# Kernel tuning notes

Hardware: AMD Instinct MI355X
Metric: run time of the kernel (lower is better)

The kernel has to match this reference:

```python
import jax, jax.numpy as jnp
import numpy as np
import math

H = 16
D_ATTN = 64
D_MID = 64
D_X = 1024
D_Z = 1024
D_OUT = 1024
B = 2
L_X = 2048
L_Z = 2048
MINUS_INFINITY = -1000000.0

def _xavier(key, shape):
    fan_in, fan_out = shape
    limit = math.sqrt(6.0 / (fan_in + fan_out))
    return jax.random.uniform(key, shape, jnp.float32, -limit, limit)

def setup_inputs() -> dict:
    key = jax.random.key(0)
    ks = jax.random.split(key, 8)
    primary = jax.random.normal(ks[0], (B, L_X, D_X), jnp.float32)
    context = jax.random.normal(ks[1], (B, L_Z, D_Z), jnp.float32)
    padding_mask = jnp.ones((B, L_Z), jnp.int32)
    # causal attention mask (b, l_x, l_z)
    attention_mask = jnp.broadcast_to(
        jnp.tril(jnp.ones((L_X, L_Z), jnp.int32))[None], (B, L_X, L_Z))
    W_qs = _xavier(ks[2], (D_X, H * D_ATTN))
    W_ks = _xavier(ks[3], (D_Z, H * D_ATTN))
    W_vs = _xavier(ks[4], (D_Z, H * D_MID))
    W_o = _xavier(ks[5], (H * D_MID, D_OUT))
    b_o = jnp.zeros((D_OUT,), jnp.float32)
    return {"primary": primary, "context": context,
            "padding_mask": padding_mask, "attention_mask": attention_mask,
            "W_qs": W_qs, "W_ks": W_ks, "W_vs": W_vs, "W_o": W_o, "b_o": b_o}

def reference(primary, context, padding_mask, attention_mask, W_qs, W_ks, W_vs, W_o, b_o):
    b, l_x, _ = primary.shape
    l_z = context.shape[1]
    # QKV projections, split into heads (head-major columns)
    q = (primary @ W_qs).reshape(b, l_x, H, D_ATTN).transpose(0, 2, 1, 3)  # (b,h,l_x,d_attn)
    k = (context @ W_ks).reshape(b, l_z, H, D_ATTN).transpose(0, 2, 1, 3)  # (b,h,l_z,d_attn)
    v = (context @ W_vs).reshape(b, l_z, H, D_MID).transpose(0, 2, 1, 3)   # (b,h,l_z,d_mid)
    scores = jnp.einsum('bhxd,bhzd->bhxz', q, k) / math.sqrt(D_ATTN)
    # combined mask: attention_mask AND padding_mask, broadcast over heads
    mask = (attention_mask * padding_mask[:, None, :])[:, None]  # (b,1,l_x,l_z)
    scores = jnp.where(mask == 0, MINUS_INFINITY, scores)
    attn = jax.nn.softmax(scores, axis=-1)
    out = jnp.einsum('bhxz,bhzm->bhxm', attn, v)  # (b,h,l_x,d_mid)
    out = out.transpose(0, 2, 1, 3).reshape(b, l_x, H * D_MID)
    return out @ W_o + b_o
```

## Files before the change

kernel.cpp:

```cpp
#include <hip/hip_runtime.h>

#define NB 2
#define LX 2048
#define LZ 2048
#define HH 16
#define DA 64
#define DM 64
#define HD 1024
#define MINF  -1000000.0f
#define QSC   0.1803368801f
#define DTHR  8.0f

typedef __attribute__((ext_vector_type(8))) short short8;
typedef __attribute__((ext_vector_type(4))) float f32x4;

static __device__ __forceinline__ ushort f2bf(float f) {
    union { float f; uint32_t u; } c; c.f = f;
    return (ushort)((c.u + 0x7FFFu + ((c.u >> 16) & 1u)) >> 16);
}

static __device__ __forceinline__ uint32_t cvtpk(float lo, float hi) {
    uint32_t r;
    asm("v_cvt_pk_bf16_f32 %0, %1, %2" : "=v"(r) : "v"(lo), "v"(hi));
    return r;
}

#define GL16(g, l) __builtin_amdgcn_global_load_lds( \
    (const __attribute__((address_space(1))) void*)(g), \
    (__attribute__((address_space(3))) void*)(l), 16, 0, 0)

__global__ __launch_bounds__(256) void cvt_both(
    const float* __restrict__ pA, const float* __restrict__ pB,
    ushort* __restrict__ oA, ushort* __restrict__ oB)
{
    const int i = blockIdx.x * 256 + threadIdx.x;
    const float* in = (i < 1048576) ? pA : pB;
    ushort* out = (i < 1048576) ? oA : oB;
    const int j = i & 1048575;
    float4 v = ((const float4*)in)[j];
    ushort4 o;
    o.x = f2bf(v.x); o.y = f2bf(v.y); o.z = f2bf(v.z); o.w = f2bf(v.w);
    ((ushort4*)out)[j] = o;
}

__global__ __launch_bounds__(256) void wtrans4(
    const float* __restrict__ W0, const float* __restrict__ W1,
    const float* __restrict__ W2, const float* __restrict__ W3,
    ushort* __restrict__ T0, ushort* __restrict__ T1,
    ushort* __restrict__ T2, ushort* __restrict__ T3)
{
    const int zz = blockIdx.z;
    const float* W = (zz == 0) ? W0 : (zz == 1) ? W1 : (zz == 2) ? W2 : W3;
    ushort* Wt = (zz == 0) ? T0 : (zz == 1) ? T1 : (zz == 2) ? T2 : T3;

    __shared__ ushort Ls[64][72];
    const int n0 = blockIdx.x * 64, k0 = blockIdx.y * 64;
    const int t = threadIdx.x;
    const int rr = t >> 4, c4 = (t & 15) * 4;
    #pragma unroll
    for (int i = 0; i < 4; ++i) {
        const int r = rr + i * 16;
        float4 v = *(const float4*)&W[(size_t)(k0 + r) * 1024 + n0 + c4];
        Ls[c4 + 0][r] = f2bf(v.x);
        Ls[c4 + 1][r] = f2bf(v.y);
        Ls[c4 + 2][r] = f2bf(v.z);
        Ls[c4 + 3][r] = f2bf(v.w);
    }
    __syncthreads();
    const int n = t >> 2, kc = (t & 3) * 16;
    *(short8*)&Wt[(size_t)(n0 + n) * 1024 + k0 + kc]     = *(const short8*)&Ls[n][kc];
    *(short8*)&Wt[(size_t)(n0 + n) * 1024 + k0 + kc + 8] = *(const short8*)&Ls[n][kc + 8];
}

template <bool OUTF32>
static __device__ __forceinline__ void gemm_body(
    const ushort* __restrict__ A, const ushort* __restrict__ Bt,
    const float* __restrict__ bias, void* __restrict__ Cout, float osc)
{
    __shared__ ushort As[128 * 32];
    __shared__ ushort Bs[128 * 32];
    const int t = threadIdx.x;
    const int w = t >> 6, l = t & 63, lr = l & 15, lg = l >> 4;
    const int wr = w >> 1, wc = w & 1;
    const int n0 = blockIdx.x * 128, m0 = blockIdx.y * 128;

    const int c0 = t, c1 = t + 256;
    const ushort* a0 = &A[(size_t)(m0 + (c0 >> 2)) * 1024 + (c0 & 3) * 8];
    const ushort* a1 = &A[(size_t)(m0 + (c1 >> 2)) * 1024 + (c1 & 3) * 8];
    const ushort* b0 = &Bt[(size_t)(n0 + (c0 >> 2)) * 1024 + (c0 & 3) * 8];
    const ushort* b1 = &Bt[(size_t)(n0 + (c1 >> 2)) * 1024 + (c1 & 3) * 8];
    ushort* lA0 = &As[w * 512];
    ushort* lA1 = &As[(4 + w) * 512];
    ushort* lB0 = &Bs[w * 512];
    ushort* lB1 = &Bs[(4 + w) * 512];

    f32x4 acc[4][4];
    #pragma unroll
    for (int i = 0; i < 4; ++i)
        #pragma unroll
        for (int j = 0; j < 4; ++j) acc[i][j] = 0.f;

    for (int k0 = 0; k0 < 1024; k0 += 32) {
        __syncthreads();
        GL16(a0 + k0, lA0);
        GL16(a1 + k0, lA1);
        GL16(b0 + k0, lB0);
        GL16(b1 + k0, lB1);
        __syncthreads();
        short8 af[4], bf[4];
        #pragma unroll
        for (int mi = 0; mi < 4; ++mi)
            af[mi] = *(const short8*)&As[(wr * 64 + mi * 16 + lr) * 32 + lg * 8];
        #pragma unroll
        for (int nj = 0; nj < 4; ++nj)
            bf[nj] = *(const short8*)&Bs[(wc * 64 + nj * 16 + lr) * 32 + lg * 8];
        #pragma unroll
        for (int mi = 0; mi < 4; ++mi)
            #pragma unroll
            for (int nj = 0; nj < 4; ++nj)
                acc[mi][nj] = __builtin_amdgcn_mfma_f32_16x16x32_bf16(
                    af[mi], bf[nj], acc[mi][nj], 0, 0, 0);
    }

    const int row0 = m0 + wr * 64, col0 = n0 + wc * 64;
    #pragma unroll
    for (int mi = 0; mi < 4; ++mi)
        #pragma unroll
        for (int nj = 0; nj < 4; ++nj) {
            const int col = col0 + nj * 16 + lr;
            #pragma unroll
            for (int r = 0; r < 4; ++r) {
                const int row = row0 + mi * 16 + lg * 4 + r;
                const float v = acc[mi][nj][r];
                if (OUTF32)
                    ((float*)Cout)[(size_t)row * 1024 + col] = v + bias[col];
                else
                    ((ushort*)Cout)[(size_t)row * 1024 + col] = f2bf(v * osc);
            }
        }
}

__global__ __launch_bounds__(256) void gemm_qkv(
    const ushort* __restrict__ Pb, const ushort* __restrict__ Cb,
    const ushort* __restrict__ Wqt, const ushort* __restrict__ Wkt,
    const ushort* __restrict__ Wvt,
    ushort* __restrict__ Qb, ushort* __restrict__ Kb, ushort* __restrict__ Vb)
{
    const int z = blockIdx.z;
    const ushort* A  = (z == 0) ? Pb : Cb;
    const ushort* Bt = (z == 0) ? Wqt : (z == 1) ? Wkt : Wvt;
    ushort* C = (z == 0) ? Qb : (z == 1) ? Kb : Vb;
    const float osc = (z == 0) ? QSC : 1.0f;
    gemm_body<false>(A, Bt, nullptr, C, osc);
}

__global__ __launch_bounds__(256) void gemm_out(
    const ushort* __restrict__ A, const ushort* __restrict__ Bt,
    const float* __restrict__ bias, float* __restrict__ Cout)
{
    gemm_body<true>(A, Bt, bias, Cout, 1.0f);
}

__global__ __launch_bounds__(256) void mask_classify(
    const int* __restrict__ amask, const int* __restrict__ pmask,
    int* __restrict__ cls)
{
    const int bid = blockIdx.x;
    const int b = bid >> 10, xb = (bid >> 5) & 31, zb = bid & 31;
    const int t = threadIdx.x;
    int andv = 1, orv = 0;
    #pragma unroll
    for (int i = 0; i < 16; ++i) {
        const int e = t + i * 256;
        const int r = e >> 6, z = e & 63;
        const int m = amask[((size_t)b * LX + xb * 64 + r) * LZ + zb * 64 + z];
        const int p = pmask[(size_t)b * LZ + zb * 64 + z];
        const int v = (m != 0) & (p != 0);
        andv &= v; orv |= v;
    }
    __shared__ int sa[256];
    __shared__ int so[256];
    sa[t] = andv; so[t] = orv;
    __syncthreads();
    for (int s = 128; s > 0; s >>= 1) {
        if (t < s) { sa[t] &= sa[t + s]; so[t] |= so[t + s]; }
        __syncthreads();
    }
    if (t == 0) cls[bid] = so[0] ? (sa[0] ? 1 : 2) : 0;
}

__global__ __launch_bounds__(256) void attn_mfma(
    const ushort* __restrict__ Qg, const ushort* __restrict__ Kg,
    const ushort* __restrict__ Vg, const int* __restrict__ amask,
    const int* __restrict__ pmask, const int* __restrict__ cls,
    ushort* __restrict__ O)
{
    __shared__ ushort Ks[64 * 72];
    __shared__ ushort Vt[64 * 64];

    const int t = threadIdx.x, w = t >> 6, l = t & 63, lr = l & 15, lg = l >> 4;
    const int x = blockIdx.x, h = blockIdx.y, b = blockIdx.z;
    const int fx = (x & 1) ? 15 - (x >> 1) : (x >> 1);
    const int qb = b ? 15 - fx : fx;
    const int qw = qb * 128 + w * 32;

    short8 qf[2][2];
    #pragma unroll
    for (int mi = 0; mi < 2; ++mi)
        #pragma unroll
        for (int ks = 0; ks < 2; ++ks)
            qf[mi][ks] = *(const short8*)&Qg[(size_t)(b * LX + qw + mi * 16 + lr) * HD
                                             + h * DA + ks * 32 + lg * 8];

    float mrun[2] = {-1e30f, -1e30f}, lrun[2] = {0.f, 0.f};
    f32x4 o[2][4];
    #pragma unroll
    for (int mi = 0; mi < 2; ++mi)
        #pragma unroll
        for (int mj = 0; mj < 4; ++mj) o[mi][mj] = 0.f;

    const int kz = t >> 2, kc = (t & 3) * 16;
    const int vz = (t >> 3) * 2, vc = (t & 7) * 8;

    for (int zb = 0; zb < LZ / 64; ++zb) {
        const int cls0 = cls[b * 1024 + (qb * 2) * 32 + zb];
        const int cls1 = cls[b * 1024 + (qb * 2 + 1) * 32 + zb];
        if ((cls0 | cls1) == 0) continue;
        const int cl = (w < 2) ? cls0 : cls1;
        const int z0 = zb * 64;

        __syncthreads();
        {
            const ushort* kp = &Kg[(size_t)(b * LZ + z0 + kz) * HD + h * DA + kc];
            *(short8*)&Ks[kz * 72 + kc]     = *(const short8*)kp;
            *(short8*)&Ks[kz * 72 + kc + 8] = *(const short8*)(kp + 8);
            const ushort* vp = &Vg[(size_t)(b * LZ + z0 + vz) * HD + h * DM + vc];
            short8 v0 = *(const short8*)vp;
            short8 v1 = *(const short8*)(vp + HD);
            const int zc = vz >> 3, zo = vz & 7;
            #pragma unroll
            for (int j = 0; j < 8; ++j) {
                const int m = vc + j;
                const int idx = m * 64 + (((zc ^ m ^ (m >> 3)) & 7) << 3) + zo;
                const uint32_t pr = (uint32_t)(ushort)v0[j] | ((uint32_t)(ushort)v1[j] << 16);
                *(uint32_t*)&Vt[idx] = pr;
            }
        }
        __syncthreads();
        if (!cl) continue;

        f32x4 s[2][4];
        __builtin_amdgcn_s_setprio(1);
        #pragma unroll
        for (int nj = 0; nj < 4; ++nj) {
            const short8 kf0 = *(const short8*)&Ks[(nj * 16 + lr) * 72 + lg * 8];
            const short8 kf1 = *(const short8*)&Ks[(nj * 16 + lr) * 72 + 32 + lg * 8];
            #pragma unroll
            for (int mi = 0; mi < 2; ++mi) {
                f32x4 z4 = 0.f;
                z4 = __builtin_amdgcn_mfma_f32_16x16x32_bf16(kf0, qf[mi][0], z4, 0, 0, 0);
                z4 = __builtin_amdgcn_mfma_f32_16x16x32_bf16(kf1, qf[mi][1], z4, 0, 0, 0);
                s[mi][nj] = z4;
            }
        }
        __builtin_amdgcn_s_setprio(0);
        if (cl == 2) {
            #pragma unroll
            for (int mi = 0; mi < 2; ++mi) {
                const size_t arow = (size_t)(b * LX + qw + mi * 16 + lr) * LZ + z0;
                #pragma unroll
                for (int nj = 0; nj < 4; ++nj)
                    #pragma unroll
                    for (int r = 0; r < 4; ++r) {
                        const int z = nj * 16 + lg * 4 + r;
                        const int ok = (amask[arow + z] != 0) & (pmask[b * LZ + z0 + z] != 0);
                        if (!ok) s[mi][nj][r] = MINF;
                    }
            }
        }
        #pragma unroll
        for (int mi = 0; mi < 2; ++mi) {
            float pm = s[mi][0][0];
            #pragma unroll
            for (int nj = 0; nj < 4; ++nj)
                #pragma unroll
                for (int r = 0; r < 4; ++r) pm = fmaxf(pm, s[mi][nj][r]);
            pm = fmaxf(pm, __shfl_xor(pm, 16));
            pm = fmaxf(pm, __shfl_xor(pm, 32));
            if (__any(pm > mrun[mi] + DTHR)) {
                const float mn = fmaxf(mrun[mi], pm);
                const float al = exp2f(mrun[mi] - mn);
                mrun[mi] = mn;
                lrun[mi] *= al;
                #pragma unroll
                for (int r = 0; r < 4; ++r) {
                    const float alq = __shfl(al, (lg << 2) + r);
                    #pragma unroll
                    for (int mj = 0; mj < 4; ++mj) o[mi][mj][r] *= alq;
                }
            }
            float sum = 0.f;
            #pragma unroll
            for (int nj = 0; nj < 4; ++nj)
                #pragma unroll
                for (int r = 0; r < 4; ++r) {
                    const float p = exp2f(s[mi][nj][r] - mrun[mi]);
                    s[mi][nj][r] = p;
                    sum += p;
                }
            sum += __shfl_xor(sum, 16);
            sum += __shfl_xor(sum, 32);
            lrun[mi] += sum;
        }
        short8 pa[2][2];
        #pragma unroll
        for (int mi = 0; mi < 2; ++mi) {
            uint32_t pk01[4], pk23[4];
            #pragma unroll
            for (int nj = 0; nj < 4; ++nj) {
                pk01[nj] = cvtpk(s[mi][nj][0], s[mi][nj][1]);
                pk23[nj] = cvtpk(s[mi][nj][2], s[mi][nj][3]);
            }
            #pragma unroll
            for (int ks = 0; ks < 2; ++ks) {
                union { uint32_t d[4]; short8 v; } u;
                u.d[0] = pk01[2 * ks];
                u.d[1] = pk23[2 * ks];
                u.d[2] = pk01[2 * ks + 1];
                u.d[3] = pk23[2 * ks + 1];
                pa[mi][ks] = u.v;
            }
        }
        __builtin_amdgcn_s_setprio(1);
        #pragma unroll
        for (int mj = 0; mj < 4; ++mj) {
            const int m_ = mj * 16 + lr;
            const int xr = (m_ ^ (m_ >> 3)) & 7;
            const int czb = lg >> 1;
            const int zo = (lg & 1) * 4;
            #pragma unroll
            for (int ks = 0; ks < 2; ++ks) {
                const int clo = (ks * 4 + czb) ^ xr;
                const int chi = (ks * 4 + 2 + czb) ^ xr;
                const uint2 lo = *(const uint2*)&Vt[m_ * 64 + ((clo & 7) << 3) + zo];
                const uint2 hi = *(const uint2*)&Vt[m_ * 64 + ((chi & 7) << 3) + zo];
                union { uint32_t d[4]; short8 v; } u;
                u.d[0] = lo.x; u.d[1] = lo.y; u.d[2] = hi.x; u.d[3] = hi.y;
                #pragma unroll
                for (int mi = 0; mi < 2; ++mi)
                    o[mi][mj] = __builtin_amdgcn_mfma_f32_16x16x32_bf16(
                        pa[mi][ks], u.v, o[mi][mj], 0, 0, 0);
            }
        }
        __builtin_amdgcn_s_setprio(0);
    }

    #pragma unroll
    for (int mi = 0; mi < 2; ++mi) {
        const float linv = 1.f / lrun[mi];
        #pragma unroll
        for (int r = 0; r < 4; ++r) {
            const float iq = __shfl(linv, (lg << 2) + r);
            #pragma unroll
            for (int mj = 0; mj < 4; ++mj)
                O[(size_t)(b * LX + qw + mi * 16 + (lg << 2) + r) * HD + h * DM + mj * 16 + lr]
                    = f2bf(o[mi][mj][r] * iq);
        }
    }
}

extern "C" void kernel_launch(void* const* d_in, const int* in_sizes, int n_in,
                              void* d_out, int out_size, void* d_ws, size_t ws_size,
                              hipStream_t stream)
{
    const float* primary = (const float*)d_in[0];
    const float* context = (const float*)d_in[1];
    const int*   pmask   = (const int*)d_in[2];
    const int*   amask   = (const int*)d_in[3];
    const float* Wq      = (const float*)d_in[4];
    const float* Wk      = (const float*)d_in[5];
    const float* Wv      = (const float*)d_in[6];
    const float* Wo      = (const float*)d_in[7];
    const float* bo      = (const float*)d_in[8];
    float* out = (float*)d_out;

    char* w8 = (char*)d_ws;
    ushort* Pb  = (ushort*)(w8 + 0);
    ushort* Cb  = (ushort*)(w8 + 8388608);
    ushort* Qb  = (ushort*)(w8 + 16777216);
    ushort* Kb  = (ushort*)(w8 + 25165824);
    ushort* Vb  = (ushort*)(w8 + 33554432);
    ushort* AOb = (ushort*)(w8 + 41943040);
    ushort* Wqt = (ushort*)(w8 + 50331648);
    ushort* Wkt = (ushort*)(w8 + 52428800);
    ushort* Wvt = (ushort*)(w8 + 54525952);
    ushort* Wot = (ushort*)(w8 + 56623104);
    int*    clsp = (int*)(w8 + 58720256);

    cvt_both<<<8192, 256, 0, stream>>>(primary, context, Pb, Cb);
    wtrans4<<<dim3(16, 16, 4), 256, 0, stream>>>(Wq, Wk, Wv, Wo, Wqt, Wkt, Wvt, Wot);
    mask_classify<<<NB * 32 * 32, 256, 0, stream>>>(amask, pmask, clsp);
    gemm_qkv<<<dim3(8, 32, 3), 256, 0, stream>>>(Pb, Cb, Wqt, Wkt, Wvt, Qb, Kb, Vb);
    attn_mfma<<<dim3(16, 16, 2), 256, 0, stream>>>(Qb, Kb, Vb, amask, pmask, clsp, AOb);
    gemm_out<<<dim3(8, 32), 256, 0, stream>>>(AOb, Wot, bo, out);
}
```

Baseline: 155.1 us.

## Halve attention query tile to 64 rows per block and double grid

The attention kernel now gives each block 64 query rows (16 per wave) instead of 128, doubling the grid to 32x16x2 and adding a launch-bounds occupancy hint of 4. Each block uses one mask-classification entry, so causal skipping happens at 64x64 granularity and fewer fully masked tiles get computed. The aim is more blocks for better load balance and occupancy on the causal workload. The cost is that each K/V tile loaded into shared memory is reused by half as many query rows, roughly doubling K/V global and LDS traffic per unit of work.

```diff
diff --git a/kernel.cpp b/kernel.cpp
--- a/kernel.cpp
+++ b/kernel.cpp
@@ -189,7 +189,7 @@
     if (t == 0) cls[bid] = so[0] ? (sa[0] ? 1 : 2) : 0;
 }
 
-__global__ __launch_bounds__(256) void attn_mfma(
+__global__ __launch_bounds__(256, 4) void attn_mfma(
     const ushort* __restrict__ Qg, const ushort* __restrict__ Kg,
     const ushort* __restrict__ Vg, const int* __restrict__ amask,
     const int* __restrict__ pmask, const int* __restrict__ cls,
@@ -200,33 +200,27 @@
 
     const int t = threadIdx.x, w = t >> 6, l = t & 63, lr = l & 15, lg = l >> 4;
     const int x = blockIdx.x, h = blockIdx.y, b = blockIdx.z;
-    const int fx = (x & 1) ? 15 - (x >> 1) : (x >> 1);
-    const int qb = b ? 15 - fx : fx;
-    const int qw = qb * 128 + w * 32;
-
-    short8 qf[2][2];
-    #pragma unroll
-    for (int mi = 0; mi < 2; ++mi)
-        #pragma unroll
-        for (int ks = 0; ks < 2; ++ks)
-            qf[mi][ks] = *(const short8*)&Qg[(size_t)(b * LX + qw + mi * 16 + lr) * HD
-                                             + h * DA + ks * 32 + lg * 8];
-
-    float mrun[2] = {-1e30f, -1e30f}, lrun[2] = {0.f, 0.f};
-    f32x4 o[2][4];
-    #pragma unroll
-    for (int mi = 0; mi < 2; ++mi)
-        #pragma unroll
-        for (int mj = 0; mj < 4; ++mj) o[mi][mj] = 0.f;
+    const int fx = (x & 1) ? 31 - (x >> 1) : (x >> 1);
+    const int qb = b ? 31 - fx : fx;
+    const int qw = qb * 64 + w * 16;
+
+    short8 qf[2];
+    #pragma unroll
+    for (int ks = 0; ks < 2; ++ks)
+        qf[ks] = *(const short8*)&Qg[(size_t)(b * LX + qw + lr) * HD
+                                     + h * DA + ks * 32 + lg * 8];
+
+    float mrun = -1e30f, lrun = 0.f;
+    f32x4 o[4];
+    #pragma unroll
+    for (int mj = 0; mj < 4; ++mj) o[mj] = 0.f;
 
     const int kz = t >> 2, kc = (t & 3) * 16;
     const int vz = (t >> 3) * 2, vc = (t & 7) * 8;
 
     for (int zb = 0; zb < LZ / 64; ++zb) {
-        const int cls0 = cls[b * 1024 + (qb * 2) * 32 + zb];
-        const int cls1 = cls[b * 1024 + (qb * 2 + 1) * 32 + zb];
-        if ((cls0 | cls1) == 0) continue;
-        const int cl = (w < 2) ? cls0 : cls1;
+        const int cl = cls[b * 1024 + qb * 32 + zb];
+        if (cl == 0) continue;
         const int z0 = zb * 64;
 
         __syncthreads();
@@ -247,56 +241,48 @@
             }
         }
         __syncthreads();
-        if (!cl) continue;
-
-        f32x4 s[2][4];
+
+        f32x4 s[4];
         __builtin_amdgcn_s_setprio(1);
         #pragma unroll
         for (int nj = 0; nj < 4; ++nj) {
             const short8 kf0 = *(const short8*)&Ks[(nj * 16 + lr) * 72 + lg * 8];
             const short8 kf1 = *(const short8*)&Ks[(nj * 16 + lr) * 72 + 32 + lg * 8];
-            #pragma unroll
-            for (int mi = 0; mi < 2; ++mi) {
-                f32x4 z4 = 0.f;
-                z4 = __builtin_amdgcn_mfma_f32_16x16x32_bf16(kf0, qf[mi][0], z4, 0, 0, 0);
-                z4 = __builtin_amdgcn_mfma_f32_16x16x32_bf16(kf1, qf[mi][1], z4, 0, 0, 0);
-                s[mi][nj] = z4;
-            }
+            f32x4 z4 = 0.f;
+            z4 = __builtin_amdgcn_mfma_f32_16x16x32_bf16(kf0, qf[0], z4, 0, 0, 0);
+            z4 = __builtin_amdgcn_mfma_f32_16x16x32_bf16(kf1, qf[1], z4, 0, 0, 0);
+            s[nj] = z4;
         }
         __builtin_amdgcn_s_setprio(0);
         if (cl == 2) {
-            #pragma unroll
-            for (int mi = 0; mi < 2; ++mi) {
-                const size_t arow = (size_t)(b * LX + qw + mi * 16 + lr) * LZ + z0;
-                #pragma unroll
-                for (int nj = 0; nj < 4; ++nj)
-                    #pragma unroll
-                    for (int r = 0; r < 4; ++r) {
-                        const int z = nj * 16 + lg * 4 + r;
-                        const int ok = (amask[arow + z] != 0) & (pmask[b * LZ + z0 + z] != 0);
-                        if (!ok) s[mi][nj][r] = MINF;
-                    }
-            }
-        }
-        #pragma unroll
-        for (int mi = 0; mi < 2; ++mi) {
-            float pm = s[mi][0][0];
+            const size_t arow = (size_t)(b * LX + qw + lr) * LZ + z0;
             #pragma unroll
             for (int nj = 0; nj < 4; ++nj)
                 #pragma unroll
-                for (int r = 0; r < 4; ++r) pm = fmaxf(pm, s[mi][nj][r]);
+                for (int r = 0; r < 4; ++r) {
+                    const int z = nj * 16 + lg * 4 + r;
+                    const int ok = (amask[arow + z] != 0) & (pmask[b * LZ + z0 + z] != 0);
+                    if (!ok) s[nj][r] = MINF;
+                }
+        }
+        {
+            float pm = s[0][0];
+            #pragma unroll
+            for (int nj = 0; nj < 4; ++nj)
+                #pragma unroll
+                for (int r = 0; r < 4; ++r) pm = fmaxf(pm, s[nj][r]);
             pm = fmaxf(pm, __shfl_xor(pm, 16));
             pm = fmaxf(pm, __shfl_xor(pm, 32));
-            if (__any(pm > mrun[mi] + DTHR)) {
-                const float mn = fmaxf(mrun[mi], pm);
-                const float al = exp2f(mrun[mi] - mn);
-                mrun[mi] = mn;
-                lrun[mi] *= al;
+            if (__any(pm > mrun + DTHR)) {
+                const float mn = fmaxf(mrun, pm);
+                const float al = exp2f(mrun - mn);
+                mrun = mn;
+                lrun *= al;
                 #pragma unroll
                 for (int r = 0; r < 4; ++r) {
                     const float alq = __shfl(al, (lg << 2) + r);
                     #pragma unroll
-                    for (int mj = 0; mj < 4; ++mj) o[mi][mj][r] *= alq;
+                    for (int mj = 0; mj < 4; ++mj) o[mj][r] *= alq;
                 }
             }
             float sum = 0.f;
@@ -304,22 +290,21 @@
             for (int nj = 0; nj < 4; ++nj)
                 #pragma unroll
                 for (int r = 0; r < 4; ++r) {
-                    const float p = exp2f(s[mi][nj][r] - mrun[mi]);
-                    s[mi][nj][r] = p;
+                    const float p = exp2f(s[nj][r] - mrun);
+                    s[nj][r] = p;
                     sum += p;
                 }
             sum += __shfl_xor(sum, 16);
             sum += __shfl_xor(sum, 32);
-            lrun[mi] += sum;
-        }
-        short8 pa[2][2];
-        #pragma unroll
-        for (int mi = 0; mi < 2; ++mi) {
+            lrun += sum;
+        }
+        short8 pa[2];
+        {
             uint32_t pk01[4], pk23[4];
             #pragma unroll
             for (int nj = 0; nj < 4; ++nj) {
-                pk01[nj] = cvtpk(s[mi][nj][0], s[mi][nj][1]);
-                pk23[nj] = cvtpk(s[mi][nj][2], s[mi][nj][3]);
+                pk01[nj] = cvtpk(s[nj][0], s[nj][1]);
+                pk23[nj] = cvtpk(s[nj][2], s[nj][3]);
             }
             #pragma unroll
             for (int ks = 0; ks < 2; ++ks) {
@@ -328,7 +313,7 @@
                 u.d[1] = pk23[2 * ks];
                 u.d[2] = pk01[2 * ks + 1];
                 u.d[3] = pk23[2 * ks + 1];
-                pa[mi][ks] = u.v;
+                pa[ks] = u.v;
             }
         }
         __builtin_amdgcn_s_setprio(1);
@@ -346,26 +331,20 @@
                 const uint2 hi = *(const uint2*)&Vt[m_ * 64 + ((chi & 7) << 3) + zo];
                 union { uint32_t d[4]; short8 v; } u;
                 u.d[0] = lo.x; u.d[1] = lo.y; u.d[2] = hi.x; u.d[3] = hi.y;
-                #pragma unroll
-                for (int mi = 0; mi < 2; ++mi)
-                    o[mi][mj] = __builtin_amdgcn_mfma_f32_16x16x32_bf16(
-                        pa[mi][ks], u.v, o[mi][mj], 0, 0, 0);
+                o[mj] = __builtin_amdgcn_mfma_f32_16x16x32_bf16(pa[ks], u.v, o[mj], 0, 0, 0);
             }
         }
         __builtin_amdgcn_s_setprio(0);
     }
 
-    #pragma unroll
-    for (int mi = 0; mi < 2; ++mi) {
-        const float linv = 1.f / lrun[mi];
-        #pragma unroll
-        for (int r = 0; r < 4; ++r) {
-            const float iq = __shfl(linv, (lg << 2) + r);
-            #pragma unroll
-            for (int mj = 0; mj < 4; ++mj)
-                O[(size_t)(b * LX + qw + mi * 16 + (lg << 2) + r) * HD + h * DM + mj * 16 + lr]
-                    = f2bf(o[mi][mj][r] * iq);
-        }
+    const float linv = 1.f / lrun;
+    #pragma unroll
+    for (int r = 0; r < 4; ++r) {
+        const float iq = __shfl(linv, (lg << 2) + r);
+        #pragma unroll
+        for (int mj = 0; mj < 4; ++mj)
+            O[(size_t)(b * LX + qw + (lg << 2) + r) * HD + h * DM + mj * 16 + lr]
+                = f2bf(o[mj][r] * iq);
     }
 }
 
@@ -401,6 +380,6 @@
     wtrans4<<<dim3(16, 16, 4), 256, 0, stream>>>(Wq, Wk, Wv, Wo, Wqt, Wkt, Wvt, Wot);
     mask_classify<<<NB * 32 * 32, 256, 0, stream>>>(amask, pmask, clsp);
     gemm_qkv<<<dim3(8, 32, 3), 256, 0, stream>>>(Pb, Cb, Wqt, Wkt, Wvt, Qb, Kb, Vb);
-    attn_mfma<<<dim3(16, 16, 2), 256, 0, stream>>>(Qb, Kb, Vb, amask, pmask, clsp, AOb);
+    attn_mfma<<<dim3(32, 16, 2), 256, 0, stream>>>(Qb, Kb, Vb, amask, pmask, clsp, AOb);
     gemm_out<<<dim3(8, 32), 256, 0, stream>>>(AOb, Wot, bo, out);
 }
```

Result: faster. 139.0 us (-10.4%).

## Split attention KV range in two and merge partials inside output GEMM

Applied to the files above, without the earlier changes.

Attention now runs with the key blocks split into two interleaved halves (even/odd blocks), doubling the grid. Each half writes unnormalized partial outputs plus per-row max and sum, and block indices are remapped across XCDs. Work lists come from a ballot over the mask classes instead of per-iteration checks. A small kernel computes the merge weights, and the output GEMM combines the two partials while loading A, using smaller M tiles. This is meant to fix the load imbalance and low occupancy of causal attention, at the cost of extra partial-output traffic, an extra launch, and a second bf16 rounding of the partials.

```diff
diff --git a/kernel.cpp b/kernel.cpp
--- a/kernel.cpp
+++ b/kernel.cpp
@@ -19,6 +19,11 @@
     return (ushort)((c.u + 0x7FFFu + ((c.u >> 16) & 1u)) >> 16);
 }
 
+static __device__ __forceinline__ float bf2f(ushort u) {
+    union { uint32_t u; float f; } c; c.u = (uint32_t)u << 16;
+    return c.f;
+}
+
 static __device__ __forceinline__ uint32_t cvtpk(float lo, float hi) {
     uint32_t r;
     asm("v_cvt_pk_bf16_f32 %0, %1, %2" : "=v"(r) : "v"(lo), "v"(hi));
@@ -72,11 +77,18 @@
     *(short8*)&Wt[(size_t)(n0 + n) * 1024 + k0 + kc + 8] = *(const short8*)&Ls[n][kc + 8];
 }
 
-template <bool OUTF32>
-static __device__ __forceinline__ void gemm_body(
-    const ushort* __restrict__ A, const ushort* __restrict__ Bt,
-    const float* __restrict__ bias, void* __restrict__ Cout, float osc)
-{
+__global__ __launch_bounds__(256) void gemm_qkv(
+    const ushort* __restrict__ Pb, const ushort* __restrict__ Cb,
+    const ushort* __restrict__ Wqt, const ushort* __restrict__ Wkt,
+    const ushort* __restrict__ Wvt,
+    ushort* __restrict__ Qb, ushort* __restrict__ Kb, ushort* __restrict__ Vb)
+{
+    const int z = blockIdx.z;
+    const ushort* A  = (z == 0) ? Pb : Cb;
+    const ushort* Bt = (z == 0) ? Wqt : (z == 1) ? Wkt : Wvt;
+    ushort* Cout = (z == 0) ? Qb : (z == 1) ? Kb : Vb;
+    const float osc = (z == 0) ? QSC : 1.0f;
+
     __shared__ ushort As[128 * 32];
     __shared__ ushort Bs[128 * 32];
     const int t = threadIdx.x;
@@ -131,34 +143,9 @@
             #pragma unroll
             for (int r = 0; r < 4; ++r) {
                 const int row = row0 + mi * 16 + lg * 4 + r;
-                const float v = acc[mi][nj][r];
-                if (OUTF32)
-                    ((float*)Cout)[(size_t)row * 1024 + col] = v + bias[col];
-                else
-                    ((ushort*)Cout)[(size_t)row * 1024 + col] = f2bf(v * osc);
-            }
-        }
-}
-
-__global__ __launch_bounds__(256) void gemm_qkv(
-    const ushort* __restrict__ Pb, const ushort* __restrict__ Cb,
-    const ushort* __restrict__ Wqt, const ushort* __restrict__ Wkt,
-    const ushort* __restrict__ Wvt,
-    ushort* __restrict__ Qb, ushort* __restrict__ Kb, ushort* __restrict__ Vb)
-{
-    const int z = blockIdx.z;
-    const ushort* A  = (z == 0) ? Pb : Cb;
-    const ushort* Bt = (z == 0) ? Wqt : (z == 1) ? Wkt : Wvt;
-    ushort* C = (z == 0) ? Qb : (z == 1) ? Kb : Vb;
-    const float osc = (z == 0) ? QSC : 1.0f;
-    gemm_body<false>(A, Bt, nullptr, C, osc);
-}
-
-__global__ __launch_bounds__(256) void gemm_out(
-    const ushort* __restrict__ A, const ushort* __restrict__ Bt,
-    const float* __restrict__ bias, float* __restrict__ Cout)
-{
-    gemm_body<true>(A, Bt, bias, Cout, 1.0f);
+                Cout[(size_t)row * 1024 + col] = f2bf(acc[mi][nj][r] * osc);
+            }
+        }
 }
 
 __global__ __launch_bounds__(256) void mask_classify(
@@ -189,20 +176,50 @@
     if (t == 0) cls[bid] = so[0] ? (sa[0] ? 1 : 2) : 0;
 }
 
-__global__ __launch_bounds__(256) void attn_mfma(
+__global__ __launch_bounds__(256, 4) void attn_mfma(
     const ushort* __restrict__ Qg, const ushort* __restrict__ Kg,
     const ushort* __restrict__ Vg, const int* __restrict__ amask,
     const int* __restrict__ pmask, const int* __restrict__ cls,
-    ushort* __restrict__ O)
+    ushort* __restrict__ Op, float2* __restrict__ ml)
 {
     __shared__ ushort Ks[64 * 72];
     __shared__ ushort Vt[64 * 64];
 
     const int t = threadIdx.x, w = t >> 6, l = t & 63, lr = l & 15, lg = l >> 4;
-    const int x = blockIdx.x, h = blockIdx.y, b = blockIdx.z;
-    const int fx = (x & 1) ? 15 - (x >> 1) : (x >> 1);
+    const int flat = blockIdx.x + 16 * (blockIdx.y + 16 * blockIdx.z);
+    const int xcd = flat & 7, ii = flat >> 3;
+    const int g = xcd + 8 * (ii >> 4);
+    const int slot = ii & 15;
+    const int h = g & 15, bs = g >> 4;
+    const int b = bs & 1, sKV = bs >> 1;
+    const int fx = (slot & 1) ? 15 - (slot >> 1) : (slot >> 1);
     const int qb = b ? 15 - fx : fx;
     const int qw = qb * 128 + w * 32;
+
+    const uint32_t halfm = sKV ? 0xAAAAAAAAu : 0x55555555u;
+    const int cv = cls[b * 1024 + (qb * 2 + (l >> 5)) * 32 + (l & 31)];
+    const unsigned long long balA = __ballot(cv != 0);
+    const unsigned long long balM = __ballot(cv == 2);
+    const uint32_t uA = ((uint32_t)balA | (uint32_t)(balA >> 32)) & halfm;
+    const uint32_t aW = (uint32_t)((w < 2) ? balA : (balA >> 32)) & halfm;
+    const uint32_t mW = (uint32_t)((w < 2) ? balM : (balM >> 32)) & halfm;
+
+    const size_t obase = (size_t)((sKV * NB + b) * LX + qw) * HD + h * DM;
+    const size_t mlbase = (size_t)((sKV * NB + b) * HH + h) * LX + qw;
+    if (uA == 0) {
+        if (l < 16) {
+            ml[mlbase + l]      = make_float2(-1e30f, 0.f);
+            ml[mlbase + 16 + l] = make_float2(-1e30f, 0.f);
+        }
+        #pragma unroll
+        for (int mi = 0; mi < 2; ++mi)
+            #pragma unroll
+            for (int r = 0; r < 4; ++r)
+                #pragma unroll
+                for (int mj = 0; mj < 4; ++mj)
+                    Op[obase + (size_t)(mi * 16 + (lg << 2) + r) * HD + mj * 16 + lr] = 0;
+        return;
+    }
 
     short8 qf[2][2];
     #pragma unroll
@@ -222,11 +239,10 @@
     const int kz = t >> 2, kc = (t & 3) * 16;
     const int vz = (t >> 3) * 2, vc = (t & 7) * 8;
 
-    for (int zb = 0; zb < LZ / 64; ++zb) {
-        const int cls0 = cls[b * 1024 + (qb * 2) * 32 + zb];
-        const int cls1 = cls[b * 1024 + (qb * 2 + 1) * 32 + zb];
-        if ((cls0 | cls1) == 0) continue;
-        const int cl = (w < 2) ? cls0 : cls1;
+    uint32_t remw = uA;
+    while (remw) {
+        const int zb = __builtin_ctz(remw);
+        remw &= remw - 1;
         const int z0 = zb * 64;
 
         __syncthreads();
@@ -242,12 +258,14 @@
             for (int j = 0; j < 8; ++j) {
                 const int m = vc + j;
                 const int idx = m * 64 + (((zc ^ m ^ (m >> 3)) & 7) << 3) + zo;
-                const uint32_t pr = (uint32_t)(ushort)v0[j] | ((uint32_t)(ushort)v1[j] << 16);
-                *(uint32_t*)&Vt[idx] = pr;
-            }
-        }
-        __syncthreads();
-        if (!cl) continue;
+                *(uint32_t*)&Vt[idx] =
+                    (uint32_t)(ushort)v0[j] | ((uint32_t)(ushort)v1[j] << 16);
+            }
+        }
+        __syncthreads();
+
+        if (!((aW >> zb) & 1)) continue;
+        const bool mixed = (mW >> zb) & 1;
 
         f32x4 s[2][4];
         __builtin_amdgcn_s_setprio(1);
@@ -264,7 +282,7 @@
             }
         }
         __builtin_amdgcn_s_setprio(0);
-        if (cl == 2) {
+        if (mixed) {
             #pragma unroll
             for (int mi = 0; mi < 2; ++mi) {
                 const size_t arow = (size_t)(b * LX + qw + mi * 16 + lr) * LZ + z0;
@@ -299,18 +317,14 @@
                     for (int mj = 0; mj < 4; ++mj) o[mi][mj][r] *= alq;
                 }
             }
-            float sum = 0.f;
             #pragma unroll
             for (int nj = 0; nj < 4; ++nj)
                 #pragma unroll
                 for (int r = 0; r < 4; ++r) {
                     const float p = exp2f(s[mi][nj][r] - mrun[mi]);
                     s[mi][nj][r] = p;
-                    sum += p;
+                    lrun[mi] += p;
                 }
-            sum += __shfl_xor(sum, 16);
-            sum += __shfl_xor(sum, 32);
-            lrun[mi] += sum;
         }
         short8 pa[2][2];
         #pragma unroll
@@ -357,16 +371,104 @@
 
     #pragma unroll
     for (int mi = 0; mi < 2; ++mi) {
-        const float linv = 1.f / lrun[mi];
-        #pragma unroll
-        for (int r = 0; r < 4; ++r) {
-            const float iq = __shfl(linv, (lg << 2) + r);
+        lrun[mi] += __shfl_xor(lrun[mi], 16);
+        lrun[mi] += __shfl_xor(lrun[mi], 32);
+    }
+    if (l < 16) {
+        ml[mlbase + l]      = make_float2(mrun[0], lrun[0]);
+        ml[mlbase + 16 + l] = make_float2(mrun[1], lrun[1]);
+    }
+    #pragma unroll
+    for (int mi = 0; mi < 2; ++mi)
+        #pragma unroll
+        for (int r = 0; r < 4; ++r)
             #pragma unroll
             for (int mj = 0; mj < 4; ++mj)
-                O[(size_t)(b * LX + qw + mi * 16 + (lg << 2) + r) * HD + h * DM + mj * 16 + lr]
-                    = f2bf(o[mi][mj][r] * iq);
-        }
-    }
+                Op[obase + (size_t)(mi * 16 + (lg << 2) + r) * HD + mj * 16 + lr]
+                    = f2bf(o[mi][mj][r]);
+}
+
+__global__ __launch_bounds__(256) void mkw(
+    const float2* __restrict__ ml, float2* __restrict__ wbuf)
+{
+    const int i = blockIdx.x * 256 + threadIdx.x;
+    const int row = i >> 4, h = i & 15;
+    const int b = row >> 11, x = row & 2047;
+    const float2 a0 = ml[(b * HH + h) * LX + x];
+    const float2 a1 = ml[NB * HH * LX + (b * HH + h) * LX + x];
+    const float M = fmaxf(a0.x, a1.x);
+    const float w0 = exp2f(a0.x - M), w1 = exp2f(a1.x - M);
+    const float inv = 1.f / fmaxf(a0.y * w0 + a1.y * w1, 1e-37f);
+    wbuf[i] = make_float2(w0 * inv, w1 * inv);
+}
+
+__global__ __launch_bounds__(256) void gemm_out_fused(
+    const ushort* __restrict__ Op, const float2* __restrict__ wbuf,
+    const ushort* __restrict__ Bt, const float* __restrict__ bias,
+    float* __restrict__ Cout)
+{
+    __shared__ ushort As[64 * 32];
+    __shared__ ushort Bs[128 * 32];
+    const int t = threadIdx.x;
+    const int w = t >> 6, l = t & 63, lr = l & 15, lg = l >> 4;
+    const int wr = w >> 1, wc = w & 1;
+    const int n0 = blockIdx.x * 128, m0 = blockIdx.y * 64;
+
+    const int ra = m0 + (t >> 2), ka = (t & 3) * 8;
+    const ushort* p0 = &Op[(size_t)ra * HD + ka];
+    const ushort* p1 = p0 + (size_t)NB * LX * HD;
+    const float2* wrow = &wbuf[ra * 16];
+    const ushort* b0 = &Bt[(size_t)(n0 + (t >> 2)) * 1024 + ka];
+    const ushort* b1 = &Bt[(size_t)(n0 + 64 + (t >> 2)) * 1024 + ka];
+    ushort* lB0 = &Bs[w * 512];
+    ushort* lB1 = &Bs[(4 + w) * 512];
+
+    f32x4 acc[2][4];
+    #pragma unroll
+    for (int i = 0; i < 2; ++i)
+        #pragma unroll
+        for (int j = 0; j < 4; ++j) acc[i][j] = 0.f;
+
+    for (int k0 = 0; k0 < 1024; k0 += 32) {
+        const short8 q0 = *(const short8*)(p0 + k0);
+        const short8 q1 = *(const short8*)(p1 + k0);
+        const float2 wv = wrow[(k0 + ka) >> 6];
+        union { ushort d[8]; short8 v; } av;
+        #pragma unroll
+        for (int j = 0; j < 8; ++j)
+            av.d[j] = f2bf(bf2f((ushort)q0[j]) * wv.x + bf2f((ushort)q1[j]) * wv.y);
+        __syncthreads();
+        *(short8*)&As[t * 8] = av.v;
+        GL16(b0 + k0, lB0);
+        GL16(b1 + k0, lB1);
+        __syncthreads();
+        short8 af[2], bf[4];
+        #pragma unroll
+        for (int mi = 0; mi < 2; ++mi)
+            af[mi] = *(const short8*)&As[(wr * 32 + mi * 16 + lr) * 32 + lg * 8];
+        #pragma unroll
+        for (int nj = 0; nj < 4; ++nj)
+            bf[nj] = *(const short8*)&Bs[(wc * 64 + nj * 16 + lr) * 32 + lg * 8];
+        #pragma unroll
+        for (int mi = 0; mi < 2; ++mi)
+            #pragma unroll
+            for (int nj = 0; nj < 4; ++nj)
+                acc[mi][nj] = __builtin_amdgcn_mfma_f32_16x16x32_bf16(
+                    af[mi], bf[nj], acc[mi][nj], 0, 0, 0);
+    }
+
+    const int row0 = m0 + wr * 32, col0 = n0 + wc * 64;
+    #pragma unroll
+    for (int mi = 0; mi < 2; ++mi)
+        #pragma unroll
+        for (int nj = 0; nj < 4; ++nj) {
+            const int col = col0 + nj * 16 + lr;
+            #pragma unroll
+            for (int r = 0; r < 4; ++r) {
+                const int row = row0 + mi * 16 + lg * 4 + r;
+                Cout[(size_t)row * 1024 + col] = acc[mi][nj][r] + bias[col];
+            }
+        }
 }
 
 extern "C" void kernel_launch(void* const* d_in, const int* in_sizes, int n_in,
@@ -390,17 +492,20 @@
     ushort* Qb  = (ushort*)(w8 + 16777216);
     ushort* Kb  = (ushort*)(w8 + 25165824);
     ushort* Vb  = (ushort*)(w8 + 33554432);
-    ushort* AOb = (ushort*)(w8 + 41943040);
     ushort* Wqt = (ushort*)(w8 + 50331648);
     ushort* Wkt = (ushort*)(w8 + 52428800);
     ushort* Wvt = (ushort*)(w8 + 54525952);
     ushort* Wot = (ushort*)(w8 + 56623104);
     int*    clsp = (int*)(w8 + 58720256);
+    ushort* Op   = Pb;
+    float2* mlp  = (float2*)Wqt;
+    float2* wbuf = (float2*)Wkt;
 
     cvt_both<<<8192, 256, 0, stream>>>(primary, context, Pb, Cb);
     wtrans4<<<dim3(16, 16, 4), 256, 0, stream>>>(Wq, Wk, Wv, Wo, Wqt, Wkt, Wvt, Wot);
     mask_classify<<<NB * 32 * 32, 256, 0, stream>>>(amask, pmask, clsp);
     gemm_qkv<<<dim3(8, 32, 3), 256, 0, stream>>>(Pb, Cb, Wqt, Wkt, Wvt, Qb, Kb, Vb);
-    attn_mfma<<<dim3(16, 16, 2), 256, 0, stream>>>(Qb, Kb, Vb, amask, pmask, clsp, AOb);
-    gemm_out<<<dim3(8, 32), 256, 0, stream>>>(AOb, Wot, bo, out);
-}
+    attn_mfma<<<dim3(16, 16, 4), 256, 0, stream>>>(Qb, Kb, Vb, amask, pmask, clsp, Op, mlp);
+    mkw<<<256, 256, 0, stream>>>(mlp, wbuf);
+    gemm_out_fused<<<dim3(8, 64), 256, 0, stream>>>(Op, wbuf, Wot, bo, out);
+}
```

Result: faster. 150.1 us (-3.2%).
